# Kernel optimization log

Hardware: AMD Instinct MI355X
Metric: run time of the kernel (lower is better)

The kernel has to match this reference:

```python
import jax, jax.numpy as jnp
import numpy as np
from jax import lax

B, H, W, C = 4, 128, 128, 192
HEADS = 4
CH = C // HEADS  # head dim = 48


def setup_inputs() -> dict:
    key = jax.random.key(0)
    ks = jax.random.split(key, 5)
    x = jax.random.normal(ks[0], (B, H, W, C), dtype=jnp.float32)
    # 1x1 conv producing qkv: stored as dense [C, 3C]
    w_qkv = jax.random.normal(ks[1], (C, 3 * C), dtype=jnp.float32) * (1.0 / np.sqrt(C))
    # depthwise 3x3 conv over 3C channels: HWIO with I=1, O=3C, feature_group_count=3C
    w_dw = jax.random.normal(ks[2], (3, 3, 1, 3 * C), dtype=jnp.float32) * (1.0 / 3.0)
    # output projection 1x1 conv: dense [C, C]
    w_proj = jax.random.normal(ks[3], (C, C), dtype=jnp.float32) * (1.0 / np.sqrt(C))
    # per-head learned temperature (initialized to ones as in the source)
    temperature = jnp.ones((HEADS,), dtype=jnp.float32)
    return {"x": x, "w_qkv": w_qkv, "w_dw": w_dw, "w_proj": w_proj, "temperature": temperature}


def _l2_normalize(t):
    # tf.keras.utils.normalize: divide by L2 norm along last axis
    return t / jnp.linalg.norm(t, axis=-1, keepdims=True)


def reference(x, w_qkv, w_dw, w_proj, temperature):
    b, h, w, c = x.shape
    hw = h * w
    # 1x1 conv == dense matmul over channels
    qkv = jnp.einsum('bhwc,cd->bhwd', x, w_qkv)  # [b,h,w,3C]
    # depthwise 3x3 SAME conv
    qkv = lax.conv_general_dilated(
        qkv, w_dw, window_strides=(1, 1), padding='SAME',
        dimension_numbers=('NHWC', 'HWIO', 'NHWC'),
        feature_group_count=3 * c)
    q, k, v = jnp.split(qkv, 3, axis=-1)  # each [b,h,w,C]

    def to_heads(t):
        # b h w (heads ch) -> b heads ch (h w)
        return t.reshape(b, hw, HEADS, CH).transpose(0, 2, 3, 1)

    q = _l2_normalize(to_heads(q))  # [b,heads,ch,hw]
    k = _l2_normalize(to_heads(k))
    v = to_heads(v)

    temp = temperature.reshape(1, HEADS, 1, 1)
    attn = jnp.einsum('bncs,bnds->bncd', q, k) * temp  # [b,heads,ch,ch]
    attn = jax.nn.softmax(attn, axis=-1)
    out = jnp.einsum('bncd,bnds->bncs', attn, v)  # [b,heads,ch,hw]
    # b heads ch (h w) -> b h w (heads ch)
    out = out.transpose(0, 3, 1, 2).reshape(b, h, w, c)
    out = jnp.einsum('bhwc,cd->bhwd', out, w_proj)
    return out
```

## Files before the change

kernel.cpp:

```cpp
#include <hip/hip_runtime.h>

namespace {

constexpr int HW = 16384;
constexpr int C  = 192;
constexpr int C3 = 576;
constexpr int CH = 48;
constexpr int K  = 192;

using bf16x8 = __attribute__((ext_vector_type(8))) short;
using f32x4  = __attribute__((ext_vector_type(4))) float;

__device__ inline unsigned short f2bf(float f) {
  unsigned u = __float_as_uint(f);
  unsigned r = (u + 0x7fff + ((u >> 16) & 1)) >> 16;
  return (unsigned short)r;
}
__device__ inline float bf2f(unsigned short b) {
  return __uint_as_float(((unsigned)b) << 16);
}
__device__ inline float4 ld_bf4(const unsigned short* p) {
  const ushort4 u = *(const ushort4*)p;
  return make_float4(bf2f(u.x), bf2f(u.y), bf2f(u.z), bf2f(u.w));
}

__device__ __forceinline__ void ld_g2l16(const unsigned short* g, unsigned short* l) {
  __builtin_amdgcn_global_load_lds(
      (const __attribute__((address_space(1))) unsigned int*)(unsigned long long)(const void*)g,
      (__attribute__((address_space(3))) unsigned int*)(unsigned int)(unsigned long long)(void*)l,
      16, 0, 0);
}

__global__ __launch_bounds__(256) void cvt_wqkv(const float* __restrict__ wqkv,
                                                unsigned short* __restrict__ wqh) {
  const int t = blockIdx.x * 256 + threadIdx.x;
  const int n = t / 192;
  const int k = t % 192;
  wqh[n * 192 + k] = f2bf(wqkv[k * C3 + n]);
}

template <int NT, bool PERB, bool OBF16, bool CVTA>
__global__ __launch_bounds__(256) void gemm_mfma(const void* __restrict__ Ap,
                                                 const unsigned short* __restrict__ Bh,
                                                 void* __restrict__ Co) {
  constexpr int N = NT * 64;
  constexpr int AST = CVTA ? 40 : 32;
  constexpr int CST = 72;
  __shared__ __align__(16) unsigned short sA[128 * AST];
  __shared__ __align__(16) unsigned short sB[2][6][64 * 32];
  __shared__ __align__(16) unsigned short sC[OBF16 ? 128 * CST : 8];
  const int t = threadIdx.x;
  const int lane = t & 63;
  const int wv = t >> 6;
  const int m0 = blockIdx.x * 128;
  const size_t boff = PERB ? (size_t)(m0 >> 14) * (192 * 192) : 0;
  const int wr = wv >> 1, wc = wv & 1;
  const int fr_row = lane & 15;
  const int fr_swz = ((lane >> 4) ^ (lane & 3)) << 3;
  const int arow0 = wv * 32;
  const int lrow  = lane >> 2;
  const int lslot = lane & 3;
  const int brow0 = wv * 16;
  const int ssl   = lslot ^ (lrow & 3);

  bf16x8 fah[6][4];
#pragma unroll
  for (int ks = 0; ks < 6; ++ks) {
    const int k0 = ks * 32;
#pragma unroll
    for (int r = 0; r < 2; ++r) {
      const int row = arow0 + r * 16 + lrow;
      if constexpr (CVTA) {
        const float* src = &((const float*)Ap)[(size_t)(m0 + row) * K + k0 + (lslot << 3)];
        const float4 f0 = *(const float4*)src;
        const float4 f1 = *(const float4*)(src + 4);
        bf16x8 h;
        h[0] = (short)f2bf(f0.x); h[1] = (short)f2bf(f0.y);
        h[2] = (short)f2bf(f0.z); h[3] = (short)f2bf(f0.w);
        h[4] = (short)f2bf(f1.x); h[5] = (short)f2bf(f1.y);
        h[6] = (short)f2bf(f1.z); h[7] = (short)f2bf(f1.w);
        const int sphys = lslot ^ (row & 3);
        *(bf16x8*)&sA[row * AST + (sphys << 3)] = h;
      } else {
        const size_t go = (size_t)(m0 + row) * K + k0 + ((lslot ^ (row & 3)) << 3);
        ld_g2l16(&((const unsigned short*)Ap)[go], &sA[(arow0 + r * 16) * AST]);
      }
    }
    __syncthreads();
#pragma unroll
    for (int i = 0; i < 4; ++i) {
      const int row = wr * 64 + i * 16 + fr_row;
      fah[ks][i] = *(const bf16x8*)&sA[row * AST + fr_swz];
    }
    __syncthreads();
  }

  auto stageB = [&](int buf, int nt_) {
#pragma unroll
    for (int s = 0; s < 6; ++s) {
      const size_t go = boff + (size_t)(nt_ * 64 + brow0 + lrow) * K + s * 32 + (ssl << 3);
      ld_g2l16(&Bh[go], &sB[buf][s][brow0 * 32]);
    }
  };

  stageB(0, 0);
  __syncthreads();
  const int er = (lane >> 4) << 2;
  const int ec = lane & 15;
  for (int nt = 0; nt < NT; ++nt) {
    const int buf = nt & 1;
    if (nt < NT - 1) stageB(buf ^ 1, nt + 1);
    f32x4 acc[4][2] = {};
#pragma unroll
    for (int ks = 0; ks < 6; ++ks) {
      bf16x8 fbh[2];
#pragma unroll
      for (int j = 0; j < 2; ++j) {
        const int row = wc * 32 + j * 16 + fr_row;
        fbh[j] = *(const bf16x8*)&sB[buf][ks][row * 32 + fr_swz];
      }
#pragma unroll
      for (int i = 0; i < 4; ++i)
#pragma unroll
        for (int j = 0; j < 2; ++j)
          acc[i][j] = __builtin_amdgcn_mfma_f32_16x16x32_bf16(fah[ks][i], fbh[j], acc[i][j], 0, 0, 0);
    }
    if constexpr (OBF16) {
#pragma unroll
      for (int i = 0; i < 4; ++i)
#pragma unroll
        for (int j = 0; j < 2; ++j)
#pragma unroll
          for (int r = 0; r < 4; ++r)
            sC[(wr * 64 + i * 16 + er + r) * CST + wc * 32 + j * 16 + ec] = f2bf(acc[i][j][r]);
      __syncthreads();
#pragma unroll
      for (int it = 0; it < 4; ++it) {
        const int idx = t + it * 256;
        const int row = idx >> 3, seg = idx & 7;
        *(bf16x8*)&((unsigned short*)Co)[(size_t)(m0 + row) * N + nt * 64 + seg * 8] =
            *(const bf16x8*)&sC[row * CST + seg * 8];
      }
    } else {
#pragma unroll
      for (int i = 0; i < 4; ++i)
#pragma unroll
        for (int j = 0; j < 2; ++j) {
          const size_t base = (size_t)(m0 + wr * 64 + i * 16 + er) * N + nt * 64 + wc * 32 + j * 16 + ec;
          float* cp = (float*)Co + base;
#pragma unroll
          for (int r = 0; r < 4; ++r) cp[(size_t)r * N] = acc[i][j][r];
        }
    }
    if (nt < NT - 1) __syncthreads();
  }
}

constexpr int TY = 8;
__global__ __launch_bounds__(256) void dwconv3x3_v6(const unsigned short* __restrict__ in,
                                                    const float* __restrict__ wdw,
                                                    unsigned short* __restrict__ qk,
                                                    unsigned short* __restrict__ vh) {
  const int t = blockIdx.x * 256 + threadIdx.x;
  const int c4 = t % 144;
  const int rest = t / 144;
  const int x = rest & 127;
  const int ys = (rest >> 7) & 15;
  const int img = rest >> 11;
  const int y0 = ys * TY;

  float4 wt[3][3];
#pragma unroll
  for (int i = 0; i < 3; ++i)
#pragma unroll
    for (int j = 0; j < 3; ++j)
      wt[i][j] = *(const float4*)&wdw[(size_t)(i * 3 + j) * C3 + c4 * 4];

  const bool xm = x > 0, xp = x < 127;
  const unsigned short* ibase = &in[((size_t)((img << 14) + x)) * C3 + c4 * 4];
  const float4 z4 = make_float4(0.f, 0.f, 0.f, 0.f);
  const ptrdiff_t dxm = xm ? -(ptrdiff_t)C3 : 0;
  const ptrdiff_t dxp = xp ? (ptrdiff_t)C3 : 0;

  auto ldrow = [&](int yy, float4* r) {
    if ((unsigned)yy < 128u) {
      const unsigned short* rp = ibase + (size_t)yy * (128 * C3);
      float4 a = ld_bf4(rp + dxm);
      float4 m = ld_bf4(rp);
      float4 b = ld_bf4(rp + dxp);
      if (!xm) a = z4;
      if (!xp) b = z4;
      r[0] = a; r[1] = m; r[2] = b;
    } else {
      r[0] = z4; r[1] = z4; r[2] = z4;
    }
  };

  float4 r0[3], r1[3], r2[3];
  float4 pf[2][3];
  ldrow(y0 - 1, r0);
  ldrow(y0, r1);
  ldrow(y0 + 1, r2);
  ldrow(y0 + 2, pf[0]);

#pragma unroll
  for (int i = 0; i < TY; ++i) {
    if (i < TY - 2) ldrow(y0 + i + 3, pf[(i + 1) & 1]);
    float4 o = z4;
#pragma unroll
    for (int j = 0; j < 3; ++j) {
      o.x += r0[j].x * wt[0][j].x; o.y += r0[j].y * wt[0][j].y;
      o.z += r0[j].z * wt[0][j].z; o.w += r0[j].w * wt[0][j].w;
      o.x += r1[j].x * wt[1][j].x; o.y += r1[j].y * wt[1][j].y;
      o.z += r1[j].z * wt[1][j].z; o.w += r1[j].w * wt[1][j].w;
      o.x += r2[j].x * wt[2][j].x; o.y += r2[j].y * wt[2][j].y;
      o.z += r2[j].z * wt[2][j].z; o.w += r2[j].w * wt[2][j].w;
    }
    const int p = (img << 14) + ((y0 + i) << 7) + x;
    const ushort4 ob = make_ushort4(f2bf(o.x), f2bf(o.y), f2bf(o.z), f2bf(o.w));
    if (c4 < 96) *(ushort4*)&qk[(size_t)p * 384 + c4 * 4] = ob;
    else         *(ushort4*)&vh[(size_t)p * 192 + (c4 - 96) * 4] = ob;
    if (i < TY - 1) {
#pragma unroll
      for (int j = 0; j < 3; ++j) { r0[j] = r1[j]; r1[j] = r2[j]; r2[j] = pf[i & 1][j]; }
    }
  }
}

__global__ __launch_bounds__(256) void gram48_v4(const unsigned short* __restrict__ qk,
                                                 float* __restrict__ G,
                                                 float* __restrict__ ssqq,
                                                 float* __restrict__ ssqk) {
  constexpr int W = 50;
  __shared__ unsigned int smem[9216];
  const int tid = threadIdx.x;
  const int lane = tid & 63;
  const int wv = tid >> 6;
  const int pair = blockIdx.y;
  const int img = pair >> 2, h = pair & 3;

  f32x4 acc[3][3] = {};
  float ssq_acc = 0.f;
  const int sch = tid % 96;
  const int shalf = tid / 96;

  for (int rnd = 0; rnd < 2; ++rnd) {
    const int sbase = (img << 14) + blockIdx.x * 256 + rnd * 128;
#pragma unroll
    for (int r = 0; r < 6; ++r) {
      const int idx = tid + (r << 8);
      const int row = idx / 12, part = idx % 12;
      const bool isq = part < 6;
      const int sub = isq ? part : part - 6;
      const uint4 v = *(const uint4*)&qk[(size_t)(sbase + row) * 384 + (isq ? 0 : 192) + h * 48 + sub * 8];
      *(uint4*)&smem[row * W + (isq ? 0 : 24) + sub * 4] = v;
    }
    __syncthreads();
    {
      const int s0 = wv * 32 + ((lane >> 4) << 3);
      const int cm = lane & 15;
      const int half = cm & 1;
      bf16x8 qf[3], kf[3];
#pragma unroll
      for (int t3 = 0; t3 < 3; ++t3) {
        const int qc = t3 * 8 + (cm >> 1);
#pragma unroll
        for (int j = 0; j < 8; ++j) {
          const unsigned uq = smem[(s0 + j) * W + qc];
          const unsigned uk = smem[(s0 + j) * W + 24 + qc];
          qf[t3][j] = (short)(half ? (uq >> 16) : (uq & 0xffffu));
          kf[t3][j] = (short)(half ? (uk >> 16) : (uk & 0xffffu));
        }
      }
#pragma unroll
      for (int mt = 0; mt < 3; ++mt)
#pragma unroll
        for (int nt = 0; nt < 3; ++nt)
          acc[mt][nt] = __builtin_amdgcn_mfma_f32_16x16x32_bf16(qf[mt], kf[nt], acc[mt][nt], 0, 0, 0);
    }
    if (tid < 192) {
      const int cu = (sch < 48) ? (sch >> 1) : 24 + ((sch - 48) >> 1);
      const int hf = sch & 1;
      const int sstart = shalf * 64;
#pragma unroll 4
      for (int s = 0; s < 64; ++s) {
        const unsigned u = smem[(sstart + s) * W + cu];
        const float v = bf2f((unsigned short)(hf ? (u >> 16) : (u & 0xffffu)));
        ssq_acc += v * v;
      }
    }
    __syncthreads();
  }

  float* red = (float*)smem;
  const int col = lane & 15;
  const int rbase = (lane >> 4) * 4;
#pragma unroll
  for (int mt = 0; mt < 3; ++mt)
#pragma unroll
    for (int nt = 0; nt < 3; ++nt)
#pragma unroll
      for (int rg = 0; rg < 4; ++rg)
        red[wv * 2304 + (mt * 16 + rbase + rg) * 48 + nt * 16 + col] = acc[mt][nt][rg];
  __syncthreads();
  float* Gm = &G[(size_t)pair * 2304];
#pragma unroll
  for (int c = 0; c < 9; ++c) {
    const int cell = tid + (c << 8);
    const float s4 = red[cell] + red[2304 + cell] + red[4608 + cell] + red[6912 + cell];
    atomicAdd(&Gm[cell], s4);
  }
  if (tid < 192) {
    if (sch < 48) atomicAdd(&ssqq[img * 192 + h * 48 + sch], ssq_acc);
    else          atomicAdd(&ssqk[img * 192 + h * 48 + sch - 48], ssq_acc);
  }
}

__global__ __launch_bounds__(64) void attn_softmax(const float* __restrict__ G,
                                                   const float* __restrict__ ssqq,
                                                   const float* __restrict__ ssqk,
                                                   const float* __restrict__ temp,
                                                   float* __restrict__ attn) {
  const int r = blockIdx.x;
  const int h = blockIdx.y & 3;
  const int img = blockIdx.y >> 2;
  const int lane = threadIdx.x;
  const size_t base = (size_t)(img * 4 + h) * 2304;
  const float t = temp[h];
  const float qn = ssqq[img * 192 + h * CH + r];
  float val = -1e30f;
  if (lane < 48) {
    const float kn = ssqk[img * 192 + h * CH + lane];
    val = G[base + r * 48 + lane] * t * rsqrtf(qn * kn);
  }
  float m = val;
#pragma unroll
  for (int off = 32; off; off >>= 1) m = fmaxf(m, __shfl_xor(m, off));
  const float e = (lane < 48) ? expf(val - m) : 0.f;
  float ssum = e;
#pragma unroll
  for (int off = 32; off; off >>= 1) ssum += __shfl_xor(ssum, off);
  if (lane < 48) attn[base + r * 48 + lane] = e / ssum;
}

__global__ __launch_bounds__(256) void make_weff(const float* __restrict__ attn,
                                                 const float* __restrict__ wproj,
                                                 unsigned short* __restrict__ weh) {
  const int t = blockIdx.x * 256 + threadIdx.x;
  const int img = t / 36864;
  const int r = t % 36864;
  const int n = r / 192;
  const int D = r % 192;
  const int h = D / 48, dd = D % 48;
  const float* A = &attn[(size_t)(img * 4 + h) * 2304 + dd];
  const float* Wp = &wproj[(size_t)(h * 48) * 192 + n];
  float acc = 0.f;
#pragma unroll
  for (int c = 0; c < 48; ++c) acc += A[c * 48] * Wp[c * 192];
  weh[(size_t)img * 36864 + n * 192 + D] = f2bf(acc);
}

}

extern "C" void kernel_launch(void* const* d_in, const int* in_sizes, int n_in,
                              void* d_out, int out_size, void* d_ws, size_t ws_size,
                              hipStream_t stream) {
  const float* x      = (const float*)d_in[0];
  const float* w_qkv  = (const float*)d_in[1];
  const float* w_dw   = (const float*)d_in[2];
  const float* w_proj = (const float*)d_in[3];
  const float* temp   = (const float*)d_in[4];
  float* out = (float*)d_out;

  auto layout_bytes = [](int NI) -> size_t {
    return (size_t)NI * HW * 576 * 2
         + (size_t)NI * HW * 384 * 2
         + (size_t)NI * HW * 192 * 2
         + 221184
         + 153600
         + 147456
         + 294912;
  };
  const int NI = (ws_size >= layout_bytes(4)) ? 4 : ((ws_size >= layout_bytes(2)) ? 2 : 1);
  const int npass = 4 / NI;
  const int npix = NI * HW;

  char* p = (char*)d_ws;
  unsigned short* qkv = (unsigned short*)p; p += (size_t)npix * 576 * 2;
  unsigned short* qk = (unsigned short*)p;  p += (size_t)npix * 384 * 2;
  unsigned short* vh = (unsigned short*)p;  p += (size_t)npix * 192 * 2;
  unsigned short* wqh = (unsigned short*)p; p += 221184;
  float* G    = (float*)p;           p += 147456;
  float* ssqq = (float*)p;           p += 3072;
  float* ssqk = (float*)p;           p += 3072;
  float* attnb = (float*)p;          p += 147456;
  unsigned short* weh = (unsigned short*)p;

  cvt_wqkv<<<432, 256, 0, stream>>>(w_qkv, wqh);
  hipMemsetAsync(G, 0, 153600, stream);

  for (int pass = 0; pass < npass; ++pass) {
    const float* xb = x + (size_t)pass * npix * K;
    float* outb = out + (size_t)pass * npix * C;
    float* Gp    = G + (size_t)pass * NI * 4 * 2304;
    float* sqp   = ssqq + (size_t)pass * NI * 192;
    float* skp   = ssqk + (size_t)pass * NI * 192;
    float* ap    = attnb + (size_t)pass * NI * 4 * 2304;
    unsigned short* wehp = weh + (size_t)pass * NI * 36864;
    gemm_mfma<9, false, true, true><<<npix / 128, 256, 0, stream>>>(
        xb, wqh, qkv);
    dwconv3x3_v6<<<npix * 144 / TY / 256, 256, 0, stream>>>(qkv, w_dw, qk, vh);
    gram48_v4<<<dim3(64, 4 * NI), 256, 0, stream>>>(qk, Gp, sqp, skp);
    attn_softmax<<<dim3(48, 4 * NI), 64, 0, stream>>>(Gp, sqp, skp, temp, ap);
    make_weff<<<NI * 144, 256, 0, stream>>>(ap, w_proj, wehp);
    gemm_mfma<3, true, false, false><<<npix / 128, 256, 0, stream>>>(
        vh, wehp, outb);
  }
}
```

Baseline: 118.5 us.

## Fuse softmax with effective-weight build and swizzle dwconv block order

Replaces the separate attn_softmax and make_weff kernels with one per-(image, head) block kernel. It computes the normalized softmax in shared memory and directly produces the bf16 effective projection weights, which removes one launch and the attn buffer round trip. It also remaps dwconv block indices in an 8-way interleave, likely to spread concurrent blocks across channel/row regions for cache or channel locality. The tradeoff is that the fused kernel runs only 16 blocks, so each block does much more serial work (36 iterations of a 48-term dot product) with low parallelism.

```diff
diff --git a/kernel.cpp b/kernel.cpp
--- a/kernel.cpp
+++ b/kernel.cpp
@@ -157,11 +157,13 @@
 }
 
 constexpr int TY = 8;
-__global__ __launch_bounds__(256) void dwconv3x3_v6(const unsigned short* __restrict__ in,
+__global__ __launch_bounds__(256) void dwconv3x3_v7(const unsigned short* __restrict__ in,
                                                     const float* __restrict__ wdw,
                                                     unsigned short* __restrict__ qk,
                                                     unsigned short* __restrict__ vh) {
-  const int t = blockIdx.x * 256 + threadIdx.x;
+  const int cpx = gridDim.x >> 3;
+  const int bid = (blockIdx.x & 7) * cpx + (blockIdx.x >> 3);
+  const int t = bid * 256 + threadIdx.x;
   const int c4 = t % 144;
   const int rest = t / 144;
   const int x = rest & 127;
@@ -316,48 +318,55 @@
   }
 }
 
-__global__ __launch_bounds__(64) void attn_softmax(const float* __restrict__ G,
-                                                   const float* __restrict__ ssqq,
-                                                   const float* __restrict__ ssqk,
-                                                   const float* __restrict__ temp,
-                                                   float* __restrict__ attn) {
-  const int r = blockIdx.x;
-  const int h = blockIdx.y & 3;
-  const int img = blockIdx.y >> 2;
-  const int lane = threadIdx.x;
-  const size_t base = (size_t)(img * 4 + h) * 2304;
-  const float t = temp[h];
-  const float qn = ssqq[img * 192 + h * CH + r];
-  float val = -1e30f;
-  if (lane < 48) {
-    const float kn = ssqk[img * 192 + h * CH + lane];
-    val = G[base + r * 48 + lane] * t * rsqrtf(qn * kn);
-  }
-  float m = val;
-#pragma unroll
-  for (int off = 32; off; off >>= 1) m = fmaxf(m, __shfl_xor(m, off));
-  const float e = (lane < 48) ? expf(val - m) : 0.f;
-  float ssum = e;
-#pragma unroll
-  for (int off = 32; off; off >>= 1) ssum += __shfl_xor(ssum, off);
-  if (lane < 48) attn[base + r * 48 + lane] = e / ssum;
-}
-
-__global__ __launch_bounds__(256) void make_weff(const float* __restrict__ attn,
-                                                 const float* __restrict__ wproj,
-                                                 unsigned short* __restrict__ weh) {
-  const int t = blockIdx.x * 256 + threadIdx.x;
-  const int img = t / 36864;
-  const int r = t % 36864;
-  const int n = r / 192;
-  const int D = r % 192;
-  const int h = D / 48, dd = D % 48;
-  const float* A = &attn[(size_t)(img * 4 + h) * 2304 + dd];
-  const float* Wp = &wproj[(size_t)(h * 48) * 192 + n];
-  float acc = 0.f;
-#pragma unroll
-  for (int c = 0; c < 48; ++c) acc += A[c * 48] * Wp[c * 192];
-  weh[(size_t)img * 36864 + n * 192 + D] = f2bf(acc);
+__global__ __launch_bounds__(256) void softmax_weff(const float* __restrict__ G,
+                                                    const float* __restrict__ ssqq,
+                                                    const float* __restrict__ ssqk,
+                                                    const float* __restrict__ temp,
+                                                    const float* __restrict__ wproj,
+                                                    unsigned short* __restrict__ weh) {
+  __shared__ float sAtt[2304];
+  __shared__ float rowM[48], rowI[48];
+  const int tid = threadIdx.x;
+  const int pair = blockIdx.x;
+  const int img = pair >> 2, h = pair & 3;
+  const float tp = temp[h];
+  const float* Gm = &G[(size_t)pair * 2304];
+#pragma unroll
+  for (int it = 0; it < 9; ++it) {
+    const int idx = tid + it * 256;
+    const int r = idx / 48, c = idx % 48;
+    const float qn = ssqq[img * 192 + h * 48 + r];
+    const float kn = ssqk[img * 192 + h * 48 + c];
+    sAtt[idx] = Gm[idx] * tp * rsqrtf(qn) * rsqrtf(kn);
+  }
+  __syncthreads();
+  if (tid < 48) {
+    float m = -1e30f;
+    for (int c = 0; c < 48; ++c) m = fmaxf(m, sAtt[tid * 48 + c]);
+    float s = 0.f;
+    for (int c = 0; c < 48; ++c) s += expf(sAtt[tid * 48 + c] - m);
+    rowM[tid] = m;
+    rowI[tid] = 1.f / s;
+  }
+  __syncthreads();
+#pragma unroll
+  for (int it = 0; it < 9; ++it) {
+    const int idx = tid + it * 256;
+    const int r = idx / 48;
+    sAtt[idx] = expf(sAtt[idx] - rowM[r]) * rowI[r];
+  }
+  __syncthreads();
+  unsigned short* wout = &weh[(size_t)img * 36864];
+#pragma unroll
+  for (int it = 0; it < 36; ++it) {
+    const int idx = tid + it * 256;
+    const int n = idx / 48, dd = idx % 48;
+    float acc = 0.f;
+#pragma unroll
+    for (int c = 0; c < 48; ++c)
+      acc += sAtt[c * 48 + dd] * wproj[(size_t)(h * 48 + c) * 192 + n];
+    wout[n * 192 + h * 48 + dd] = f2bf(acc);
+  }
 }
 
 }
@@ -378,7 +387,6 @@
          + (size_t)NI * HW * 192 * 2
          + 221184
          + 153600
-         + 147456
          + 294912;
   };
   const int NI = (ws_size >= layout_bytes(4)) ? 4 : ((ws_size >= layout_bytes(2)) ? 2 : 1);
@@ -393,7 +401,6 @@
   float* G    = (float*)p;           p += 147456;
   float* ssqq = (float*)p;           p += 3072;
   float* ssqk = (float*)p;           p += 3072;
-  float* attnb = (float*)p;          p += 147456;
   unsigned short* weh = (unsigned short*)p;
 
   cvt_wqkv<<<432, 256, 0, stream>>>(w_qkv, wqh);
@@ -405,14 +412,12 @@
     float* Gp    = G + (size_t)pass * NI * 4 * 2304;
     float* sqp   = ssqq + (size_t)pass * NI * 192;
     float* skp   = ssqk + (size_t)pass * NI * 192;
-    float* ap    = attnb + (size_t)pass * NI * 4 * 2304;
     unsigned short* wehp = weh + (size_t)pass * NI * 36864;
     gemm_mfma<9, false, true, true><<<npix / 128, 256, 0, stream>>>(
         xb, wqh, qkv);
-    dwconv3x3_v6<<<npix * 144 / TY / 256, 256, 0, stream>>>(qkv, w_dw, qk, vh);
+    dwconv3x3_v7<<<npix * 144 / TY / 256, 256, 0, stream>>>(qkv, w_dw, qk, vh);
     gram48_v4<<<dim3(64, 4 * NI), 256, 0, stream>>>(qk, Gp, sqp, skp);
-    attn_softmax<<<dim3(48, 4 * NI), 64, 0, stream>>>(Gp, sqp, skp, temp, ap);
-    make_weff<<<NI * 144, 256, 0, stream>>>(ap, w_proj, wehp);
+    softmax_weff<<<NI * 4, 256, 0, stream>>>(Gp, sqp, skp, temp, w_proj, wehp);
     gemm_mfma<3, true, false, false><<<npix / 128, 256, 0, stream>>>(
         vh, wehp, outb);
   }
```

Result: slower. 139.5 us (+17.8%).
